# Kernel optimization log

Hardware: AMD Instinct MI355X
Metric: run time of the kernel (lower is better)

Reference implementation:

```python
import jax, jax.numpy as jnp
import numpy as np

N = 4096      # nodes
E = 65536     # edges
BAG = 16      # bloom indices per node
BF = 8192     # bloom_filter_dim (padding_idx == BF)
CIN = 128     # in_channels
HID = 512     # hidden_channels
G = 64        # num graphs
ALPHA = 0.2   # PPR teleport prob


def _prelu(z, a):
    return jnp.where(z >= 0, z, a * z)


def _mlp(x, W1, b1, W2, b2, W3, b3, a1, a2, a3, Ws, bs):
    h = _prelu(x @ W1 + b1, a1)
    h = _prelu(h @ W2 + b2, a2)
    h = _prelu(h @ W3 + b3, a3)
    return h + x @ Ws + bs


def setup_inputs() -> dict:
    key = jax.random.key(0)
    ks = iter(jax.random.split(key, 48))
    rn = lambda shape, s=0.05: jax.random.normal(next(ks), shape, dtype=jnp.float32) * s
    z = lambda *s: jnp.zeros(s, jnp.float32)
    inp = {}
    inp['codebook'] = rn((BF + 1, CIN)).at[BF].set(0.0)  # padding row zero
    # GCN tower 1
    inp['g1_W0'] = rn((CIN, HID)); inp['g1_b0'] = z(HID)
    inp['g1_W1'] = rn((HID, HID)); inp['g1_b1'] = z(HID)
    inp['g1_a'] = jnp.full((HID,), 0.25, jnp.float32)
    # GCN tower 2 (diffusion view)
    inp['g2_W0'] = rn((CIN, HID)); inp['g2_b0'] = z(HID)
    inp['g2_W1'] = rn((HID, HID)); inp['g2_b1'] = z(HID)
    inp['g2_a'] = jnp.full((HID,), 0.25, jnp.float32)
    # MLP1 (local, HID->HID)
    inp['m1_W1'] = rn((HID, HID)); inp['m1_b1'] = z(HID)
    inp['m1_W2'] = rn((HID, HID)); inp['m1_b2'] = z(HID)
    inp['m1_W3'] = rn((HID, HID)); inp['m1_b3'] = z(HID)
    inp['m1_a1'] = jnp.float32(0.25); inp['m1_a2'] = jnp.float32(0.25); inp['m1_a3'] = jnp.float32(0.25)
    inp['m1_Ws'] = rn((HID, HID)); inp['m1_bs'] = z(HID)
    # MLP2 (global, 2*HID -> HID)
    inp['m2_W1'] = rn((2 * HID, HID)); inp['m2_b1'] = z(HID)
    inp['m2_W2'] = rn((HID, HID)); inp['m2_b2'] = z(HID)
    inp['m2_W3'] = rn((HID, HID)); inp['m2_b3'] = z(HID)
    inp['m2_a1'] = jnp.float32(0.25); inp['m2_a2'] = jnp.float32(0.25); inp['m2_a3'] = jnp.float32(0.25)
    inp['m2_Ws'] = rn((2 * HID, HID)); inp['m2_bs'] = z(HID)
    inp['x_idx'] = jax.random.randint(next(ks), (N, BAG), 0, BF)
    inp['edge_index'] = jax.random.randint(next(ks), (2, E), 0, N)
    inp['batch'] = jnp.sort(jax.random.randint(next(ks), (N,), 0, G))
    return inp


def reference(codebook,
              g1_W0, g1_b0, g1_W1, g1_b1, g1_a,
              g2_W0, g2_b0, g2_W1, g2_b1, g2_a,
              m1_W1, m1_b1, m1_W2, m1_b2, m1_W3, m1_b3, m1_a1, m1_a2, m1_a3, m1_Ws, m1_bs,
              m2_W1, m2_b1, m2_W2, m2_b2, m2_W3, m2_b3, m2_a1, m2_a2, m2_a3, m2_Ws, m2_bs,
              x_idx, edge_index, batch):
    # EmbeddingBag (mean mode, padding_idx=BF)
    mask = (x_idx != BF)
    emb = codebook[x_idx]                                    # [N, BAG, CIN]
    x = (emb * mask[..., None]).sum(1) / jnp.maximum(mask.sum(1)[:, None], 1).astype(emb.dtype)
    src, dst = edge_index[0], edge_index[1]
    # --- sparse GCN normalization (self-loops, symmetric norm) ---
    sl = jnp.arange(N)
    s = jnp.concatenate([src, sl]); d = jnp.concatenate([dst, sl])
    deg = jax.ops.segment_sum(jnp.ones(s.shape[0], x.dtype), d, N)
    dis = 1.0 / jnp.sqrt(jnp.maximum(deg, 1e-12))
    nrm = (dis[s] * dis[d])[:, None]
    def gcn_sparse(z, W, b):
        return jax.ops.segment_sum((z @ W)[s] * nrm, d, N) + b
    # --- PPR diffusion: S = alpha*(I - (1-alpha) * D^-1/2 (A+I) D^-1/2)^-1 ---
    I = jnp.eye(N, dtype=x.dtype)
    A = jnp.zeros((N, N), x.dtype).at[src, dst].set(1.0)
    Ah = A + I
    di = 1.0 / jnp.sqrt(Ah.sum(1))
    An = di[:, None] * Ah * di[None, :]
    S = ALPHA * jnp.linalg.solve(I - (1.0 - ALPHA) * An, I)
    # GCN normalization of the dense diffusion graph (self-loop weight 1,
    # degrees over target nodes, messages flow row(src)->col(dst))
    Sh = S + I
    dc = 1.0 / jnp.sqrt(jnp.maximum(Sh.sum(0), 1e-12))
    P = dc[:, None] * Sh.T * dc[None, :]
    def gcn_dense(z, W, b):
        return P @ (z @ W) + b
    def tower(xin, gcn_fn, W0, b0, W1, b1, a):
        z1 = _prelu(gcn_fn(xin, W0, b0), a)
        z2 = _prelu(gcn_fn(z1, W1, b1), a)
        g = jnp.concatenate([jax.ops.segment_sum(z1, batch, G),
                             jax.ops.segment_sum(z2, batch, G)], axis=1)
        return z2, g
    lv1, gv1 = tower(x, gcn_sparse, g1_W0, g1_b0, g1_W1, g1_b1, g1_a)
    lv2, gv2 = tower(x, gcn_dense, g2_W0, g2_b0, g2_W1, g2_b1, g2_a)  # PPR view keeps x unchanged
    lv1 = _mlp(lv1, m1_W1, m1_b1, m1_W2, m1_b2, m1_W3, m1_b3, m1_a1, m1_a2, m1_a3, m1_Ws, m1_bs)
    lv2 = _mlp(lv2, m1_W1, m1_b1, m1_W2, m1_b2, m1_W3, m1_b3, m1_a1, m1_a2, m1_a3, m1_Ws, m1_bs)
    gv1 = _mlp(gv1, m2_W1, m2_b1, m2_W2, m2_b2, m2_W3, m2_b3, m2_a1, m2_a2, m2_a3, m2_Ws, m2_bs)
    gv2 = _mlp(gv2, m2_W1, m2_b1, m2_W2, m2_b2, m2_W3, m2_b3, m2_a1, m2_a2, m2_a3, m2_Ws, m2_bs)
    return (lv1, gv1, lv2, gv2)
```

## Files before the change

### kernel.cpp

```cpp
#include <hip/hip_runtime.h>

#define NN 4096
#define NE 65536
#define NBAG 16
#define BFD 8192
#define CIN 128
#define HIDC 512
#define NG 64
#define ALPHA_C 0.2f
#define BETA_C 0.8f
#define K_CH 10
#define K_W 10

typedef unsigned short u16;
typedef __attribute__((ext_vector_type(8))) short short8;
typedef __attribute__((ext_vector_type(4))) short short4v;
typedef __attribute__((ext_vector_type(4))) float f32x4;
typedef __attribute__((ext_vector_type(2))) float f32x2;

__device__ __forceinline__ short f2bf(float f){
  unsigned u = __float_as_uint(f);
  u += 0x7fffu + ((u >> 16) & 1u);
  return (short)(u >> 16);
}
__device__ __forceinline__ float bf2f(u16 h){
  return __uint_as_float(((unsigned)h) << 16);
}
__device__ __forceinline__ void gload16(const void* g, const void* l){
  __builtin_amdgcn_global_load_lds(
    (const __attribute__((address_space(1))) unsigned int*)g,
    (__attribute__((address_space(3))) unsigned int*)l, 16, 0, 0);
}

__global__ void k_prep0(const float* __restrict__ cb, const int* __restrict__ xidx,
                        float* __restrict__ xf, u16* __restrict__ xfbf,
                        const int* __restrict__ ei, unsigned* __restrict__ Ab,
                        unsigned* __restrict__ ATb, int* __restrict__ cntD,
                        const int* __restrict__ batch, int* __restrict__ bcnt){
  int bx = blockIdx.x;
  if (bx < 2048){
    int n = bx*2 + (threadIdx.x >> 7);
    int c = threadIdx.x & 127;
    float acc = 0.f; int cnt = 0;
    #pragma unroll
    for (int b = 0; b < NBAG; ++b){
      int id = xidx[n*NBAG + b];
      if (id != BFD){ acc += cb[(size_t)id*CIN + c]; ++cnt; }
    }
    float v = acc / (float)(cnt > 0 ? cnt : 1);
    xf[(size_t)n*CIN + c] = v;
    xfbf[(size_t)n*CIN + c] = (u16)f2bf(v);
  } else if (bx < 2304){
    int e = (bx - 2048)*256 + threadIdx.x;
    int s = ei[e], d = ei[NE + e];
    atomicOr(&Ab[s*128 + (d >> 5)], 1u << (d & 31));
    atomicOr(&ATb[d*128 + (s >> 5)], 1u << (s & 31));
    atomicAdd(&cntD[d], 1);
  } else {
    int n = (bx - 2304)*256 + threadIdx.x;
    if (n < NN) atomicAdd(&bcnt[batch[n]], 1);
  }
}

__global__ void k_popc2(const unsigned* __restrict__ Ab, const unsigned* __restrict__ ATb,
                        float* __restrict__ di, int* __restrict__ cntAT){
  int wid = (blockIdx.x*blockDim.x + threadIdx.x) >> 6;
  int lane = threadIdx.x & 63;
  if (wid >= 2*NN) return;
  const unsigned* bits; int r;
  if (wid < NN){ bits = Ab; r = wid; }
  else { bits = ATb; r = wid - NN; }
  int s = __popc(bits[r*128 + lane]) + __popc(bits[r*128 + 64 + lane]);
  #pragma unroll
  for (int off = 32; off > 0; off >>= 1) s += __shfl_down(s, off);
  if (lane == 0){
    if (wid < NN) di[r] = rsqrtf((float)s + 1.0f);
    else cntAT[r] = s;
  }
}

__global__ void k_prefix3(const int* __restrict__ c0, int* __restrict__ r0, int n0,
                          const int* __restrict__ c1, int* __restrict__ r1, int n1,
                          const int* __restrict__ c2, int* __restrict__ r2, int n2,
                          float* __restrict__ dis){
  const int* cnt; int* rp; int n;
  if (blockIdx.x == 0){ cnt = c0; rp = r0; n = n0; }
  else if (blockIdx.x == 1){ cnt = c1; rp = r1; n = n1; }
  else { cnt = c2; rp = r2; n = n2; }
  __shared__ int a[4096];
  __shared__ int ps[1024];
  int t = threadIdx.x;
  for (int i = t; i < 4096; i += 1024) a[i] = (i < n) ? cnt[i] : 0;
  __syncthreads();
  if (blockIdx.x == 1){
    for (int i = t; i < NN; i += 1024) dis[i] = rsqrtf((float)a[i] + 1.0f);
  }
  int b0 = a[t*4], b1 = a[t*4+1], b2 = a[t*4+2], b3 = a[t*4+3];
  int s0 = b0, s1 = s0+b1, s2 = s1+b2, s3 = s2+b3;
  ps[t] = s3;
  __syncthreads();
  for (int off = 1; off < 1024; off <<= 1){
    int v = ps[t];
    int u = (t >= off) ? ps[t-off] : 0;
    __syncthreads();
    ps[t] = v + u;
    __syncthreads();
  }
  int excl = (t > 0) ? ps[t-1] : 0;
  int base = t*4;
  if (base     < n) rp[base]   = excl;
  if (base + 1 < n) rp[base+1] = excl + s0;
  if (base + 2 < n) rp[base+2] = excl + s1;
  if (base + 3 < n) rp[base+3] = excl + s2;
  if (t == 1023) rp[n] = ps[1023];
}

struct WDesc { const float* src; u16* dst; int K; int N; };
struct WPack { WDesc w[12]; };

__global__ void k_fillwconv(const unsigned* __restrict__ bits, const int* __restrict__ rpA,
                            int* __restrict__ colidx,
                            const int* __restrict__ ei, const int* __restrict__ rpD,
                            int* __restrict__ cur, int* __restrict__ srcs,
                            WPack p){
  int bx = blockIdx.x;
  if (bx < 1024){
    int wid = (bx*blockDim.x + threadIdx.x) >> 6;
    int lane = threadIdx.x & 63;
    unsigned w0 = bits[wid*128 + lane];
    unsigned w1 = bits[wid*128 + 64 + lane];
    int c = __popc(w0) + __popc(w1);
    int x = c;
    #pragma unroll
    for (int d = 1; d < 64; d <<= 1){
      int y = __shfl_up(x, d);
      if (lane >= d) x += y;
    }
    int pos = rpA[wid] + (x - c);
    while (w0){ int b = __ffs(w0) - 1; w0 &= w0 - 1; colidx[pos++] = lane*32 + b; }
    while (w1){ int b = __ffs(w1) - 1; w1 &= w1 - 1; colidx[pos++] = (64 + lane)*32 + b; }
  } else if (bx < 1280){
    int e = (bx - 1024)*256 + threadIdx.x;
    int s = ei[e], d = ei[NE + e];
    int pos = atomicAdd(&cur[d], 1);
    srcs[rpD[d] + pos] = s;
  } else {
    int t5 = bx - 1280;
    int z = t5 >> 9;
    int rem = t5 & 511;
    int ky = rem >> 4, nx = rem & 15;
    WDesc d = p.w[z];
    int k0 = ky*32, n0 = nx*32;
    if (k0 >= d.K || n0 >= d.N) return;
    __shared__ float t[32][33];
    int tx = threadIdx.x & 31, ty = threadIdx.x >> 5;
    #pragma unroll
    for (int r = 0; r < 4; ++r){
      int row = ty + r*8;
      t[row][tx] = d.src[(size_t)(k0 + row)*d.N + n0 + tx];
    }
    __syncthreads();
    #pragma unroll
    for (int r = 0; r < 4; ++r){
      int row = ty + r*8;
      d.dst[(size_t)(n0 + row)*d.K + k0 + tx] = (u16)f2bf(t[tx][row]);
    }
  }
}

__global__ __launch_bounds__(256) void k_gcn_sp(const u16* __restrict__ U, float* __restrict__ out,
    u16* __restrict__ outbf,
    const int* __restrict__ rp, const int* __restrict__ srcs, const float* __restrict__ dis,
    const float* __restrict__ bias, const float* __restrict__ avec){
  int wid = (blockIdx.x*256 + threadIdx.x) >> 6;
  int lane = threadIdx.x & 63;
  if (wid >= NN) return;
  int j = wid;
  f32x4 a0 = {0,0,0,0}, a1 = {0,0,0,0};
  int b = rp[j], e = rp[j+1];
  for (int base = b; base < e; base += 64){
    int idx = base + lane;
    int myc = 0; float myd = 0.f;
    if (idx < e){ myc = srcs[idx]; myd = dis[myc]; }
    int m = min(64, e - base);
    for (int k = 0; k < m; ++k){
      int s = __shfl(myc, k); float w = __shfl(myd, k);
      const u16* Us = U + (size_t)s*HIDC;
      short4v q0 = *(const short4v*)(Us + lane*4);
      short4v q1 = *(const short4v*)(Us + 256 + lane*4);
      #pragma unroll
      for (int r = 0; r < 4; ++r){
        a0[r] += w*bf2f((u16)q0[r]);
        a1[r] += w*bf2f((u16)q1[r]);
      }
    }
  }
  float dj = dis[j];
  const u16* Uj = U + (size_t)j*HIDC;
  short4v s0 = *(const short4v*)(Uj + lane*4);
  short4v s1 = *(const short4v*)(Uj + 256 + lane*4);
  #pragma unroll
  for (int r = 0; r < 4; ++r){
    a0[r] += dj*bf2f((u16)s0[r]);
    a1[r] += dj*bf2f((u16)s1[r]);
  }
  float* op = out + (size_t)j*HIDC;
  u16* ob = outbf + (size_t)j*HIDC;
  #pragma unroll
  for (int v = 0; v < 4; ++v){
    int c0 = lane*4 + v, c1 = 256 + lane*4 + v;
    float x0 = dj*a0[v] + bias[c0]; float p0 = avec[c0];
    float r0 = x0 >= 0.f ? x0 : p0*x0;
    op[c0] = r0; ob[c0] = (u16)f2bf(r0);
    float x1 = dj*a1[v] + bias[c1]; float p1 = avec[c1];
    float r1 = x1 >= 0.f ? x1 : p1*x1;
    op[c1] = r1; ob[c1] = (u16)f2bf(r1);
  }
}

template<int MODE>
__global__ __launch_bounds__(256) void k_wstep(const float* __restrict__ w, const float* wp,
    float* __restrict__ wn, const int* __restrict__ rp, const int* __restrict__ cols,
    const float* __restrict__ di, float* __restrict__ dcv, float om,
    const float* __restrict__ xf, float* __restrict__ Zb128){
  int wid = (blockIdx.x*256 + threadIdx.x) >> 6;
  int lane = threadIdx.x & 63;
  if (wid >= NN) return;
  int b = rp[wid], e = rp[wid+1];
  float acc = 0.f;
  for (int k = b + lane; k < e; k += 64){
    int i = cols[k];
    float wi = (MODE == 0) ? ALPHA_C : w[i];
    acc += di[i]*wi;
  }
  #pragma unroll
  for (int o = 32; o > 0; o >>= 1) acc += __shfl_xor(acc, o);
  float dj = di[wid];
  float wj = (MODE == 0) ? ALPHA_C : w[wid];
  float basic = ALPHA_C + BETA_C*dj*(acc + dj*wj);
  float v = (MODE == 0) ? basic : (om*basic + (1.f - om)*wp[wid]);
  if (MODE == 2){
    float d2 = rsqrtf(fmaxf(v + 1.0f, 1e-12f));
    if (lane == 0) dcv[wid] = d2;
    f32x2 xv = *(const f32x2*)(xf + (size_t)wid*128 + lane*2);
    f32x2 z; z[0] = ALPHA_C*d2*xv[0]; z[1] = ALPHA_C*d2*xv[1];
    *(f32x2*)(Zb128 + (size_t)wid*128 + lane*2) = z;
  } else {
    if (lane == 0) wn[wid] = v;
  }
}

template<int FIN>
__global__ __launch_bounds__(256) void k_b128(const float* __restrict__ X, const float* __restrict__ Z,
    const float* Xp, float* Xn, u16* __restrict__ Pxbf,
    const int* __restrict__ rp, const int* __restrict__ cols,
    const float* __restrict__ di, float om,
    const float* __restrict__ dcv, const float* __restrict__ xf){
  int wid = (blockIdx.x*256 + threadIdx.x) >> 6;
  int lane = threadIdx.x & 63;
  if (wid >= NN) return;
  int j = wid;
  int b = rp[j], e = rp[j+1];
  float dj = di[j];
  f32x2 a0 = {0,0};
  for (int base = b; base < e; base += 64){
    int idx = base + lane;
    int myc = 0; float myd = 0.f;
    if (idx < e){ myc = cols[idx]; myd = di[myc]; }
    int m = min(64, e - base);
    for (int k = 0; k < m; ++k){
      int i = __shfl(myc, k); float w = __shfl(myd, k);
      a0 += w * (*(const f32x2*)(X + (size_t)i*128 + lane*2));
    }
  }
  a0 += dj * (*(const f32x2*)(X + (size_t)j*128 + lane*2));
  f32x2 basic = *(const f32x2*)(Z + (size_t)j*128 + lane*2) + (BETA_C*dj)*a0;
  f32x2 xp = *(const f32x2*)(Xp + (size_t)j*128 + lane*2);
  f32x2 v; v[0] = om*basic[0] + (1.f-om)*xp[0]; v[1] = om*basic[1] + (1.f-om)*xp[1];
  if constexpr (FIN){
    float d2 = dcv[j];
    f32x2 fv = *(const f32x2*)(xf + (size_t)j*128 + lane*2);
    unsigned pk = (unsigned)(unsigned short)f2bf(d2*(v[0] + d2*fv[0]))
                | ((unsigned)(unsigned short)f2bf(d2*(v[1] + d2*fv[1])) << 16);
    *(unsigned*)(Pxbf + (size_t)j*128 + lane*2) = pk;
  } else {
    *(f32x2*)(Xn + (size_t)j*128 + lane*2) = v;
  }
}

template<int FIN>
__global__ __launch_bounds__(256) void k_b512d(const float* __restrict__ X, const float* __restrict__ Z,
    const float* Xp, float* Xn, u16* __restrict__ Xnbf,
    const int* __restrict__ rp, const int* __restrict__ cols,
    const float* __restrict__ di, float om,
    const float* __restrict__ dcv, const u16* __restrict__ Ubf,
    const float* __restrict__ bias, const float* __restrict__ avec){
  int wid = (blockIdx.x*256 + threadIdx.x) >> 6;
  int lane = threadIdx.x & 63;
  if (wid >= NN) return;
  int b = rp[wid], e = rp[wid+1];
  float dj = di[wid];
  const int co0 = lane*4, co1 = 256 + lane*4;
  f32x4 a0 = {0,0,0,0}, a1 = {0,0,0,0};
  for (int base = b; base < e; base += 64){
    int idx = base + lane;
    int myc = 0; float myd = 0.f;
    if (idx < e){ myc = cols[idx]; myd = di[myc]; }
    int m = min(64, e - base);
    for (int k = 0; k < m; ++k){
      int i = __shfl(myc, k); float w = __shfl(myd, k);
      const float* Xi = X + (size_t)i*512;
      a0 += w * (*(const f32x4*)(Xi + co0));
      a1 += w * (*(const f32x4*)(Xi + co1));
    }
  }
  const float* Xj = X + (size_t)wid*512;
  a0 += dj * (*(const f32x4*)(Xj + co0));
  a1 += dj * (*(const f32x4*)(Xj + co1));
  const float* Zj = Z + (size_t)wid*512;
  f32x4 b0 = *(const f32x4*)(Zj + co0) + (BETA_C*dj)*a0;
  f32x4 b1 = *(const f32x4*)(Zj + co1) + (BETA_C*dj)*a1;
  const float* Pj = Xp + (size_t)wid*512;
  f32x4 p0 = *(const f32x4*)(Pj + co0);
  f32x4 p1 = *(const f32x4*)(Pj + co1);
  f32x4 v0, v1;
  #pragma unroll
  for (int q = 0; q < 4; ++q){
    v0[q] = om*b0[q] + (1.f-om)*p0[q];
    v1[q] = om*b1[q] + (1.f-om)*p1[q];
  }
  if constexpr (FIN){
    float d2 = dcv[wid];
    const u16* Uj = Ubf + (size_t)wid*512;
    short4v pk0, pk1;
    #pragma unroll
    for (int q = 0; q < 4; ++q){
      float x0 = d2*(v0[q] + d2*bf2f(Uj[co0 + q])) + bias[co0 + q];
      float pa0 = avec[co0 + q];
      float r0 = x0 >= 0.f ? x0 : pa0*x0;
      v0[q] = r0; pk0[q] = f2bf(r0);
      float x1 = d2*(v1[q] + d2*bf2f(Uj[co1 + q])) + bias[co1 + q];
      float pa1 = avec[co1 + q];
      float r1 = x1 >= 0.f ? x1 : pa1*x1;
      v1[q] = r1; pk1[q] = f2bf(r1);
    }
    float* oj = Xn + (size_t)wid*512;
    u16* bj = Xnbf + (size_t)wid*512;
    *(f32x4*)(oj + co0) = v0;
    *(f32x4*)(oj + co1) = v1;
    *(short4v*)(bj + co0) = pk0;
    *(short4v*)(bj + co1) = pk1;
  } else {
    float* oj = Xn + (size_t)wid*512;
    *(f32x4*)(oj + co0) = v0;
    *(f32x4*)(oj + co1) = v1;
  }
}

__global__ void k_segsum(const float* __restrict__ z1, const float* __restrict__ z2,
                         const int* __restrict__ gptr, u16* __restrict__ gv){
  int g = blockIdx.x, t = threadIdx.x;
  float s0 = 0, s1 = 0, s2 = 0, s3 = 0;
  int rb = gptr[g], re = gptr[g+1];
  for (int r = rb; r < re; ++r){
    s0 += z1[(size_t)r*HIDC + t];       s1 += z1[(size_t)r*HIDC + 256 + t];
    s2 += z2[(size_t)r*HIDC + t];       s3 += z2[(size_t)r*HIDC + 256 + t];
  }
  gv[g*1024 + t] = (u16)f2bf(s0); gv[g*1024 + 256 + t] = (u16)f2bf(s1);
  gv[g*1024 + 512 + t] = (u16)f2bf(s2); gv[g*1024 + 768 + t] = (u16)f2bf(s3);
}

template<int BM, int BN, int ACT, int ADDM, int BIAS, int KC, int SPLIT, int ZOUT, int WF32, int WBF, int DUAL>
__global__ __launch_bounds__(256, 2) void k_gemm(
    const u16* __restrict__ A, const u16* __restrict__ Bt,
    float* __restrict__ C, u16* __restrict__ Cb,
    const float* __restrict__ bias, const float* __restrict__ ap,
    const float* __restrict__ addm, float* __restrict__ C2,
    float* __restrict__ zb, const float* __restrict__ dcv,
    const float* __restrict__ bias2, const float* __restrict__ ap2,
    int M, int Nn, int K)
{
  __shared__ __align__(16) u16 As[2][BM*32];
  __shared__ __align__(16) u16 Bs[2][BN*32];
  const int tid = threadIdx.x;
  int nwg = gridDim.x * gridDim.y;
  int flat = blockIdx.y * gridDim.x + blockIdx.x;
  int swz = (flat & 7) * (nwg >> 3) + (flat >> 3);
  int bxx = swz % gridDim.x, byy = swz / gridDim.x;
  const int bm0 = byy*BM, bn0 = bxx*BN;
  const int lane = tid & 63, wv = tid >> 6;
  const int wr = wv >> 1, wc = wv & 1;
  constexpr int MR = BM/32, NR = BN/32;
  f32x4 acc[MR][NR];
  #pragma unroll
  for (int i = 0; i < MR; ++i)
    #pragma unroll
    for (int j = 0; j < NR; ++j) acc[i][j] = (f32x4){0.f,0.f,0.f,0.f};
  const int r0 = wr*(BM/2), c0 = wc*(BN/2);
  const int glr = lane >> 2, glc = (lane & 3)*8;
  int k0 = 0, k1 = K;
  if constexpr (KC > 0){ k0 = blockIdx.z*KC; k1 = k0 + KC; }
  const int nt = (k1 - k0) >> 5;
  auto STAGE = [&](int buf, int kt){
    #pragma unroll
    for (int q = 0; q < BM/64; ++q)
      gload16(A + (size_t)(bm0 + q*64 + wv*16 + glr)*K + kt + glc, &As[buf][(q*4+wv)*512]);
    #pragma unroll
    for (int q = 0; q < BN/64; ++q)
      gload16(Bt + (size_t)(bn0 + q*64 + wv*16 + glr)*K + kt + glc, &Bs[buf][(q*4+wv)*512]);
  };
  STAGE(0, k0);
  __syncthreads();
  for (int t = 0; t < nt; ++t){
    if (t + 1 < nt) STAGE((t+1)&1, k0 + ((t+1) << 5));
    short8 af[MR], bfv[NR];
    #pragma unroll
    for (int mi = 0; mi < MR; ++mi)
      af[mi] = *(const short8*)&As[t&1][(r0 + mi*16 + (lane & 15))*32 + (lane >> 4)*8];
    #pragma unroll
    for (int ni = 0; ni < NR; ++ni)
      bfv[ni] = *(const short8*)&Bs[t&1][(c0 + ni*16 + (lane & 15))*32 + (lane >> 4)*8];
    #pragma unroll
    for (int mi = 0; mi < MR; ++mi)
      #pragma unroll
      for (int ni = 0; ni < NR; ++ni)
        acc[mi][ni] = __builtin_amdgcn_mfma_f32_16x16x32_bf16(af[mi], bfv[ni], acc[mi][ni], 0, 0, 0);
    __syncthreads();
  }
  #pragma unroll
  for (int mi = 0; mi < MR; ++mi){
    #pragma unroll
    for (int ni = 0; ni < NR; ++ni){
      int col = bn0 + c0 + ni*16 + (lane & 15);
      #pragma unroll
      for (int q = 0; q < 4; ++q){
        int row = bm0 + r0 + mi*16 + ((lane >> 4) << 2) + q;
        float v = acc[mi][ni][q];
        if constexpr (KC > 0){
          C[(size_t)blockIdx.z*M*Nn + (size_t)row*Nn + col] = v;
        } else if constexpr (DUAL){
          if (col < 512){
            v += bias[col];
            C[(size_t)row*512 + col] = v;
          } else {
            int c2 = col - 512;
            v += bias2[c2];
            float a = ap2[0];
            v = v >= 0.f ? v : a*v;
            Cb[(size_t)row*512 + c2] = (u16)f2bf(v);
          }
        } else {
          if constexpr (BIAS) v += bias[col];
          if constexpr (ACT == 1){ float a = ap[col]; v = v >= 0.f ? v : a*v; }
          if constexpr (ACT == 2){ float a = ap[0];   v = v >= 0.f ? v : a*v; }
          if constexpr (ADDM) v += addm[(size_t)row*Nn + col];
          if constexpr (WF32){
            if constexpr (SPLIT){
              float* dst = (row < NN) ? (C + (size_t)row*Nn) : (C2 + (size_t)(row - NN)*Nn);
              dst[col] = v;
            } else {
              C[(size_t)row*Nn + col] = v;
            }
          }
          if constexpr (WBF) Cb[(size_t)row*Nn + col] = (u16)f2bf(v);
          if constexpr (ZOUT) zb[(size_t)row*Nn + col] = ALPHA_C * dcv[row] * v;
        }
      }
    }
  }
}

template<int MODE>
__global__ void k_red(const float* __restrict__ part, int KS, int Nn,
                      const float* __restrict__ b1, const float* __restrict__ a1s,
                      const float* __restrict__ b2, const float* __restrict__ a2s,
                      float* __restrict__ Cf, u16* __restrict__ Cb,
                      const float* __restrict__ addm,
                      float* __restrict__ o1, float* __restrict__ o2){
  int idx = blockIdx.x*256 + threadIdx.x;
  if (idx >= 128*Nn) return;
  float v = 0.f;
  for (int z = 0; z < KS; ++z) v += part[(size_t)z*128*Nn + idx];
  int row = idx / Nn, col = idx - row*Nn;
  if constexpr (MODE == 0){
    if (col < 512){
      v += b1[col];
      Cf[(size_t)row*512 + col] = v;
    } else {
      int c2 = col - 512;
      v += b2[c2];
      float a = a2s[0]; v = v >= 0.f ? v : a*v;
      Cb[(size_t)row*512 + c2] = (u16)f2bf(v);
    }
  } else if constexpr (MODE == 1){
    v += b1[col];
    float a = a1s[0]; v = v >= 0.f ? v : a*v;
    Cb[idx] = (u16)f2bf(v);
  } else {
    v += b1[col];
    float a = a1s[0]; v = v >= 0.f ? v : a*v;
    v += addm[idx];
    if (row < NG) o1[(size_t)row*Nn + col] = v;
    else o2[(size_t)(row - NG)*Nn + col] = v;
  }
}

extern "C" void kernel_launch(void* const* d_in, const int* in_sizes, int n_in,
                              void* d_out, int out_size, void* d_ws, size_t ws_size,
                              hipStream_t stream) {
  const float* cb   = (const float*)d_in[0];
  const float* g1W0 = (const float*)d_in[1];  const float* g1b0 = (const float*)d_in[2];
  const float* g1W1 = (const float*)d_in[3];  const float* g1b1 = (const float*)d_in[4];
  const float* g1a  = (const float*)d_in[5];
  const float* g2W0 = (const float*)d_in[6];  const float* g2b0 = (const float*)d_in[7];
  const float* g2W1 = (const float*)d_in[8];  const float* g2b1 = (const float*)d_in[9];
  const float* g2a  = (const float*)d_in[10];
  const float* m1W1 = (const float*)d_in[11]; const float* m1b1 = (const float*)d_in[12];
  const float* m1W2 = (const float*)d_in[13]; const float* m1b2 = (const float*)d_in[14];
  const float* m1W3 = (const float*)d_in[15]; const float* m1b3 = (const float*)d_in[16];
  const float* m1a1 = (const float*)d_in[17]; const float* m1a2 = (const float*)d_in[18];
  const float* m1a3 = (const float*)d_in[19];
  const float* m1Ws = (const float*)d_in[20]; const float* m1bs = (const float*)d_in[21];
  const float* m2W1 = (const float*)d_in[22]; const float* m2b1 = (const float*)d_in[23];
  const float* m2W2 = (const float*)d_in[24]; const float* m2b2 = (const float*)d_in[25];
  const float* m2W3 = (const float*)d_in[26]; const float* m2b3 = (const float*)d_in[27];
  const float* m2a1 = (const float*)d_in[28]; const float* m2a2 = (const float*)d_in[29];
  const float* m2a3 = (const float*)d_in[30];
  const float* m2Ws = (const float*)d_in[31]; const float* m2bs = (const float*)d_in[32];
  const int* xidx  = (const int*)d_in[33];
  const int* ei    = (const int*)d_in[34];
  const int* batch = (const int*)d_in[35];
  float* out = (float*)d_out;
  char* W = (char*)d_ws;
  constexpr size_t MB = 1024u*1024u;
  constexpr size_t KB = 1024u;

  unsigned* Abits  = (unsigned*)(W);
  unsigned* ATbits = (unsigned*)(W + 2*MB);
  u16* w_g1W0t   = (u16*)(W);
  u16* w_g2W0t   = (u16*)(W + 128*KB);
  u16* w_g1W1t   = (u16*)(W + 256*KB);
  u16* w_g2W1t   = (u16*)(W + 768*KB);
  u16* w_m1WsW1t = (u16*)(W + 1280*KB);
  u16* w_m1W2t   = (u16*)(W + 2304*KB);
  u16* w_m1W3t   = (u16*)(W + 2816*KB);
  char* M4 = W + 4*MB;
  int* cntD  = (int*)(M4);
  int* cur   = (int*)(M4 + 16*KB);
  int* bcnt  = (int*)(M4 + 32*KB);
  int* cntAT = (int*)(M4 + 48*KB);
  int* rpAT  = (int*)(M4 + 80*KB);
  int* rpD   = (int*)(M4 + 100*KB);
  int* gptr  = (int*)(M4 + 120*KB);
  float* di  = (float*)(M4 + 124*KB);
  float* dis = (float*)(M4 + 140*KB);
  float* dc  = (float*)(M4 + 156*KB);
  float* wv0 = (float*)(M4 + 172*KB);
  float* wv1 = (float*)(M4 + 188*KB);
  int* colAT = (int*)(W + 4*MB + 256*KB);
  int* srcD  = (int*)(W + 4*MB + 512*KB);
  u16* gvbf  = (u16*)(W + 4*MB + 768*KB);
  u16* gh1bf = (u16*)(W + 5*MB);
  u16* gh2bf = (u16*)(W + 5*MB + 128*KB);
  float* gsb = (float*)(W + 5*MB + 256*KB);
  float* xf  = (float*)(W + 6*MB);
  u16* xfbf  = (u16*)(W + 8*MB);
  u16* PxBf  = (u16*)(W + 9*MB);
  u16* w_m2WsW1t = (u16*)(W + 10*MB);
  u16* w_m2W2t   = (u16*)(W + 12*MB);
  u16* w_m2W3t   = (u16*)(W + 12*MB + 512*KB);
  float* Zb128 = (float*)(W + 13*MB);
  float* Zb  = (float*)(W + 15*MB);
  float* XA  = (float*)(W + 23*MB);
  float* XB  = (float*)(W + 31*MB);
  u16* z1sbf = (u16*)(W + 35*MB);
  u16* Ubf   = (u16*)(W + 39*MB);
  float* z1s = (float*)(W + 43*MB);
  u16* zsbf  = (u16*)(W + 51*MB);
  u16* z21bf = zsbf;
  u16* z22bf = (u16*)(W + 55*MB);
  float* ztmp = (float*)(W + 59*MB);
  float* sb  = Zb;
  u16* h1    = (u16*)(W + 31*MB);
  u16* h2    = (u16*)(W + 59*MB);
  float* gpart = (float*)(W + 59*MB);
  float* XA128 = XA;
  float* XB128 = XB;

  float omg[11];
  {
    double o = 1.0; omg[0] = 0.f; omg[1] = 1.0f;
    for (int k = 2; k <= 10; ++k){ o = 1.0/(1.0 - 0.16*o); omg[k] = (float)o; }
  }

  hipMemsetAsync(W, 0, 4*MB, stream);
  hipMemsetAsync(M4, 0, 64*KB, stream);

  k_prep0<<<2320, 256, 0, stream>>>(cb, xidx, xf, xfbf, ei, Abits, ATbits, cntD, batch, bcnt);
  k_popc2<<<2048, 256, 0, stream>>>(Abits, ATbits, di, cntAT);
  k_prefix3<<<3, 1024, 0, stream>>>(cntAT, rpAT, NN, cntD, rpD, NN, bcnt, gptr, NG, dis);
  {
    WPack p = {{ {g1W0, w_g1W0t, 128, 512}, {g2W0, w_g2W0t, 128, 512},
                 {g1W1, w_g1W1t, 512, 512}, {g2W1, w_g2W1t, 512, 512},
                 {m1Ws, w_m1WsW1t, 512, 512}, {m1W1, w_m1WsW1t + 512*512, 512, 512},
                 {m1W2, w_m1W2t, 512, 512}, {m1W3, w_m1W3t, 512, 512},
                 {m2Ws, w_m2WsW1t, 1024, 512}, {m2W1, w_m2WsW1t + 512*1024, 1024, 512},
                 {m2W2, w_m2W2t, 512, 512}, {m2W3, w_m2W3t, 512, 512} }};
    k_fillwconv<<<1280 + 6144, 256, 0, stream>>>(ATbits, rpAT, colAT, ei, rpD, cur, srcD, p);
  }

  k_gemm<128,64,0,0,0,0,0,0,0,1,0><<<dim3(8, 32), 256, 0, stream>>>(
      xfbf, w_g1W0t, nullptr, Ubf, nullptr, nullptr, nullptr, nullptr, nullptr, nullptr, nullptr, nullptr, NN, HIDC, CIN);
  k_gcn_sp<<<1024, 256, 0, stream>>>(Ubf, z1s, z1sbf, rpD, srcD, dis, g1b0, g1a);
  k_gemm<128,64,0,0,0,0,0,0,0,1,0><<<dim3(8, 32), 256, 0, stream>>>(
      z1sbf, w_g1W1t, nullptr, Ubf, nullptr, nullptr, nullptr, nullptr, nullptr, nullptr, nullptr, nullptr, NN, HIDC, HIDC);
  k_gcn_sp<<<1024, 256, 0, stream>>>(Ubf, ztmp, z21bf, rpD, srcD, dis, g1b1, g1a);
  k_segsum<<<NG, 256, 0, stream>>>(z1s, ztmp, gptr, gvbf);

  k_wstep<0><<<1024, 256, 0, stream>>>(nullptr, nullptr, wv0, rpAT, colAT, di, nullptr, 1.0f, nullptr, nullptr);
  {
    float *curp = wv0, *prv = wv0;
    for (int k = 2; k < K_W; ++k){
      float* nxt = (k == 2) ? wv1 : (float*)prv;
      if (k == 2) prv = wv0;
      k_wstep<1><<<1024, 256, 0, stream>>>(curp, prv, nxt, rpAT, colAT, di, nullptr, omg[k], nullptr, nullptr);
      float* t = curp; curp = nxt; prv = t;
    }
    k_wstep<2><<<1024, 256, 0, stream>>>(curp, prv, nullptr, rpAT, colAT, di, dc, omg[K_W], xf, Zb128);
  }

  k_b128<0><<<1024, 256, 0, stream>>>(Zb128, Zb128, Zb128, XA128, nullptr, rpAT, colAT, di, 1.0f, nullptr, nullptr);
  {
    float *curp = XA128, *prv = Zb128;
    for (int k = 2; k < K_CH; ++k){
      float* nxt = (k == 2) ? XB128 : prv;
      k_b128<0><<<1024, 256, 0, stream>>>(curp, Zb128, prv, nxt, nullptr, rpAT, colAT, di, omg[k], nullptr, nullptr);
      prv = curp; curp = nxt;
    }
    k_b128<1><<<1024, 256, 0, stream>>>(curp, Zb128, prv, nullptr, PxBf, rpAT, colAT, di, omg[K_CH], dc, xf);
  }
  k_gemm<128,64,1,0,1,0,0,0,1,1,0><<<dim3(8, 32), 256, 0, stream>>>(
      PxBf, w_g2W0t, z1s, z1sbf, g2b0, g2a, nullptr, nullptr, nullptr, nullptr, nullptr, nullptr, NN, HIDC, CIN);

  k_gemm<128,64,0,0,0,0,0,1,0,1,0><<<dim3(8, 32), 256, 0, stream>>>(
      z1sbf, w_g2W1t, nullptr, Ubf, nullptr, nullptr, nullptr, nullptr, Zb, dc, nullptr, nullptr, NN, HIDC, HIDC);
  k_b512d<0><<<1024, 256, 0, stream>>>(Zb, Zb, Zb, XA, nullptr, rpAT, colAT, di, 1.0f, nullptr, nullptr, nullptr, nullptr);
  {
    float *curp = XA, *prv = Zb;
    for (int k = 2; k < K_CH; ++k){
      float* nxt = (k == 2) ? XB : prv;
      k_b512d<0><<<1024, 256, 0, stream>>>(curp, Zb, prv, nxt, nullptr, rpAT, colAT, di, omg[k], nullptr, nullptr, nullptr, nullptr);
      prv = curp; curp = nxt;
    }
    k_b512d<1><<<1024, 256, 0, stream>>>(curp, Zb, prv, ztmp, z22bf, rpAT, colAT, di, omg[K_CH], dc, Ubf, g2b1, g2a);
  }
  k_segsum<<<NG, 256, 0, stream>>>(z1s, ztmp, gptr, gvbf + 64*1024);

  k_gemm<128,64,0,0,0,0,0,0,0,0,1><<<dim3(16, 64), 256, 0, stream>>>(
      zsbf, w_m1WsW1t, sb, h1, m1bs, nullptr, nullptr, nullptr, nullptr, nullptr, m1b1, m1a1, 8192, 1024, HIDC);
  k_gemm<128,64,2,0,1,0,0,0,0,1,0><<<dim3(8, 64), 256, 0, stream>>>(
      h1, w_m1W2t, nullptr, h2, m1b2, m1a2, nullptr, nullptr, nullptr, nullptr, nullptr, nullptr, 8192, HIDC, HIDC);
  k_gemm<128,64,2,1,1,0,1,0,1,0,0><<<dim3(8, 64), 256, 0, stream>>>(
      h2, w_m1W3t, out, nullptr, m1b3, m1a3, sb, out + 2129920, nullptr, nullptr, nullptr, nullptr, 8192, HIDC, HIDC);

  k_gemm<64,64,0,0,0,128,0,0,1,0,0><<<dim3(16, 2, 8), 256, 0, stream>>>(
      gvbf, w_m2WsW1t, gpart, nullptr, nullptr, nullptr, nullptr, nullptr, nullptr, nullptr, nullptr, nullptr, 128, 1024, 1024);
  k_red<0><<<512, 256, 0, stream>>>(gpart, 8, 1024, m2bs, nullptr, m2b1, m2a1, gsb, gh1bf, nullptr, nullptr, nullptr);
  k_gemm<64,64,0,0,0,64,0,0,1,0,0><<<dim3(8, 2, 8), 256, 0, stream>>>(
      gh1bf, w_m2W2t, gpart, nullptr, nullptr, nullptr, nullptr, nullptr, nullptr, nullptr, nullptr, nullptr, 128, HIDC, HIDC);
  k_red<1><<<256, 256, 0, stream>>>(gpart, 8, 512, m2b2, m2a2, nullptr, nullptr, nullptr, gh2bf, nullptr, nullptr, nullptr);
  k_gemm<64,64,0,0,0,64,0,0,1,0,0><<<dim3(8, 2, 8), 256, 0, stream>>>(
      gh2bf, w_m2W3t, gpart, nullptr, nullptr, nullptr, nullptr, nullptr, nullptr, nullptr, nullptr, nullptr, 128, HIDC, HIDC);
  k_red<2><<<256, 256, 0, stream>>>(gpart, 8, 512, m2b3, m2a3, nullptr, nullptr, nullptr, nullptr, gsb, out + 2097152, out + 4227072);
}
```

Measured before the change: 537.5 us.

## Store 512-wide PPR diffusion iterates in bf16 and fuse global MLP into one kernel

The 512-channel PPR/Chebyshev diffusion loop now reads and writes its neighbour-gathered iterates in bf16 instead of fp32. This halves the bandwidth of the dominant sparse gather passes, at the cost of extra rounding on every iteration. Separately, the global-view MLP, previously three split-K GEMMs plus three reduction kernels, is replaced by a single fused kernel. That kernel chains all three layers through shared memory, which removes five launches and the partial-sum round trips. Because it runs on only 8 blocks, it may underuse the GPU.

```diff
diff --git a/kernel.cpp b/kernel.cpp
--- a/kernel.cpp
+++ b/kernel.cpp
@@ -289,8 +289,8 @@
 }
 
 template<int FIN>
-__global__ __launch_bounds__(256) void k_b512d(const float* __restrict__ X, const float* __restrict__ Z,
-    const float* Xp, float* Xn, u16* __restrict__ Xnbf,
+__global__ __launch_bounds__(256) void k_b512h(const u16* __restrict__ X, const float* __restrict__ Z,
+    const u16* Xp, u16* Xn, float* __restrict__ zo, u16* __restrict__ zobf,
     const int* __restrict__ rp, const int* __restrict__ cols,
     const float* __restrict__ di, float om,
     const float* __restrict__ dcv, const u16* __restrict__ Ubf,
@@ -309,25 +309,37 @@
     int m = min(64, e - base);
     for (int k = 0; k < m; ++k){
       int i = __shfl(myc, k); float w = __shfl(myd, k);
-      const float* Xi = X + (size_t)i*512;
-      a0 += w * (*(const f32x4*)(Xi + co0));
-      a1 += w * (*(const f32x4*)(Xi + co1));
-    }
-  }
-  const float* Xj = X + (size_t)wid*512;
-  a0 += dj * (*(const f32x4*)(Xj + co0));
-  a1 += dj * (*(const f32x4*)(Xj + co1));
+      const u16* Xi = X + (size_t)i*512;
+      short4v x0 = *(const short4v*)(Xi + co0);
+      short4v x1 = *(const short4v*)(Xi + co1);
+      #pragma unroll
+      for (int q = 0; q < 4; ++q){
+        a0[q] += w*bf2f((u16)x0[q]);
+        a1[q] += w*bf2f((u16)x1[q]);
+      }
+    }
+  }
+  {
+    const u16* Xj = X + (size_t)wid*512;
+    short4v x0 = *(const short4v*)(Xj + co0);
+    short4v x1 = *(const short4v*)(Xj + co1);
+    #pragma unroll
+    for (int q = 0; q < 4; ++q){
+      a0[q] += dj*bf2f((u16)x0[q]);
+      a1[q] += dj*bf2f((u16)x1[q]);
+    }
+  }
   const float* Zj = Z + (size_t)wid*512;
   f32x4 b0 = *(const f32x4*)(Zj + co0) + (BETA_C*dj)*a0;
   f32x4 b1 = *(const f32x4*)(Zj + co1) + (BETA_C*dj)*a1;
-  const float* Pj = Xp + (size_t)wid*512;
-  f32x4 p0 = *(const f32x4*)(Pj + co0);
-  f32x4 p1 = *(const f32x4*)(Pj + co1);
+  const u16* Pj = Xp + (size_t)wid*512;
+  short4v p0 = *(const short4v*)(Pj + co0);
+  short4v p1 = *(const short4v*)(Pj + co1);
   f32x4 v0, v1;
   #pragma unroll
   for (int q = 0; q < 4; ++q){
-    v0[q] = om*b0[q] + (1.f-om)*p0[q];
-    v1[q] = om*b1[q] + (1.f-om)*p1[q];
+    v0[q] = om*b0[q] + (1.f-om)*bf2f((u16)p0[q]);
+    v1[q] = om*b1[q] + (1.f-om)*bf2f((u16)p1[q]);
   }
   if constexpr (FIN){
     float d2 = dcv[wid];
@@ -344,16 +356,19 @@
       float r1 = x1 >= 0.f ? x1 : pa1*x1;
       v1[q] = r1; pk1[q] = f2bf(r1);
     }
-    float* oj = Xn + (size_t)wid*512;
-    u16* bj = Xnbf + (size_t)wid*512;
+    float* oj = zo + (size_t)wid*512;
+    u16* bj = zobf + (size_t)wid*512;
     *(f32x4*)(oj + co0) = v0;
     *(f32x4*)(oj + co1) = v1;
     *(short4v*)(bj + co0) = pk0;
     *(short4v*)(bj + co1) = pk1;
   } else {
-    float* oj = Xn + (size_t)wid*512;
-    *(f32x4*)(oj + co0) = v0;
-    *(f32x4*)(oj + co1) = v1;
+    short4v w0, w1;
+    #pragma unroll
+    for (int q = 0; q < 4; ++q){ w0[q] = f2bf(v0[q]); w1[q] = f2bf(v1[q]); }
+    u16* oj = Xn + (size_t)wid*512;
+    *(short4v*)(oj + co0) = w0;
+    *(short4v*)(oj + co1) = w1;
   }
 }
 
@@ -370,13 +385,125 @@
   gv[g*1024 + 512 + t] = (u16)f2bf(s2); gv[g*1024 + 768 + t] = (u16)f2bf(s3);
 }
 
+__global__ __launch_bounds__(512) void k_mlp2(
+    const u16* __restrict__ gv, const u16* __restrict__ wsw1,
+    const u16* __restrict__ w2t, const u16* __restrict__ w3t,
+    const float* __restrict__ bs, const float* __restrict__ b1,
+    const float* __restrict__ b2, const float* __restrict__ b3,
+    const float* __restrict__ a1s, const float* __restrict__ a2s,
+    const float* __restrict__ a3s,
+    float* __restrict__ o1, float* __restrict__ o2)
+{
+  __shared__ __align__(16) u16 Ar[16*1032];
+  __shared__ float gsb_s[16*512];
+  __shared__ __align__(16) u16 h1_s[16*520];
+  __shared__ __align__(16) u16 h2_s[16*520];
+  int tid = threadIdx.x;
+  int wv = tid >> 6, lane = tid & 63;
+  int row0 = blockIdx.x * 16;
+  for (int c = tid; c < 2048; c += 512){
+    int r = c >> 7, i = (c & 127)*8;
+    *(short8*)&Ar[r*1032 + i] = *(const short8*)&gv[(size_t)(row0 + r)*1024 + i];
+  }
+  __syncthreads();
+  const int fr = lane & 15, fq = lane >> 4;
+  {
+    f32x4 acc[8];
+    #pragma unroll
+    for (int t = 0; t < 8; ++t) acc[t] = (f32x4){0,0,0,0};
+    for (int ks = 0; ks < 32; ++ks){
+      short8 af = *(const short8*)&Ar[fr*1032 + ks*32 + fq*8];
+      #pragma unroll
+      for (int t = 0; t < 8; ++t){
+        int n = (wv*8 + t)*16 + fr;
+        short8 bfv = *(const short8*)&wsw1[(size_t)n*1024 + ks*32 + fq*8];
+        acc[t] = __builtin_amdgcn_mfma_f32_16x16x32_bf16(af, bfv, acc[t], 0, 0, 0);
+      }
+    }
+    #pragma unroll
+    for (int t = 0; t < 8; ++t){
+      int n = (wv*8 + t)*16 + fr;
+      #pragma unroll
+      for (int q = 0; q < 4; ++q){
+        int r = fq*4 + q;
+        float v = acc[t][q];
+        if (n < 512){
+          gsb_s[r*512 + n] = v + bs[n];
+        } else {
+          float x = v + b1[n - 512];
+          float a = a1s[0];
+          x = x >= 0.f ? x : a*x;
+          h1_s[r*520 + (n - 512)] = (u16)f2bf(x);
+        }
+      }
+    }
+  }
+  __syncthreads();
+  {
+    f32x4 acc[4];
+    #pragma unroll
+    for (int t = 0; t < 4; ++t) acc[t] = (f32x4){0,0,0,0};
+    for (int ks = 0; ks < 16; ++ks){
+      short8 af = *(const short8*)&h1_s[fr*520 + ks*32 + fq*8];
+      #pragma unroll
+      for (int t = 0; t < 4; ++t){
+        int n = (wv*4 + t)*16 + fr;
+        short8 bfv = *(const short8*)&w2t[(size_t)n*512 + ks*32 + fq*8];
+        acc[t] = __builtin_amdgcn_mfma_f32_16x16x32_bf16(af, bfv, acc[t], 0, 0, 0);
+      }
+    }
+    #pragma unroll
+    for (int t = 0; t < 4; ++t){
+      int n = (wv*4 + t)*16 + fr;
+      #pragma unroll
+      for (int q = 0; q < 4; ++q){
+        int r = fq*4 + q;
+        float x = acc[t][q] + b2[n];
+        float a = a2s[0];
+        x = x >= 0.f ? x : a*x;
+        h2_s[r*520 + n] = (u16)f2bf(x);
+      }
+    }
+  }
+  __syncthreads();
+  {
+    f32x4 acc[4];
+    #pragma unroll
+    for (int t = 0; t < 4; ++t) acc[t] = (f32x4){0,0,0,0};
+    for (int ks = 0; ks < 16; ++ks){
+      short8 af = *(const short8*)&h2_s[fr*520 + ks*32 + fq*8];
+      #pragma unroll
+      for (int t = 0; t < 4; ++t){
+        int n = (wv*4 + t)*16 + fr;
+        short8 bfv = *(const short8*)&w3t[(size_t)n*512 + ks*32 + fq*8];
+        acc[t] = __builtin_amdgcn_mfma_f32_16x16x32_bf16(af, bfv, acc[t], 0, 0, 0);
+      }
+    }
+    #pragma unroll
+    for (int t = 0; t < 4; ++t){
+      int n = (wv*4 + t)*16 + fr;
+      #pragma unroll
+      for (int q = 0; q < 4; ++q){
+        int r = fq*4 + q;
+        float x = acc[t][q] + b3[n];
+        float a = a3s[0];
+        x = x >= 0.f ? x : a*x;
+        x += gsb_s[r*512 + n];
+        int grow = row0 + r;
+        if (grow < NG) o1[(size_t)grow*512 + n] = x;
+        else o2[(size_t)(grow - NG)*512 + n] = x;
+      }
+    }
+  }
+}
+
 template<int BM, int BN, int ACT, int ADDM, int BIAS, int KC, int SPLIT, int ZOUT, int WF32, int WBF, int DUAL>
 __global__ __launch_bounds__(256, 2) void k_gemm(
     const u16* __restrict__ A, const u16* __restrict__ Bt,
     float* __restrict__ C, u16* __restrict__ Cb,
     const float* __restrict__ bias, const float* __restrict__ ap,
     const float* __restrict__ addm, float* __restrict__ C2,
-    float* __restrict__ zb, const float* __restrict__ dcv,
+    float* __restrict__ zb, u16* __restrict__ zbh, const float* __restrict__ dcv,
     const float* __restrict__ bias2, const float* __restrict__ ap2,
     int M, int Nn, int K)
 {
@@ -463,45 +590,14 @@
             }
           }
           if constexpr (WBF) Cb[(size_t)row*Nn + col] = (u16)f2bf(v);
-          if constexpr (ZOUT) zb[(size_t)row*Nn + col] = ALPHA_C * dcv[row] * v;
+          if constexpr (ZOUT){
+            float zv = ALPHA_C * dcv[row] * v;
+            zb[(size_t)row*Nn + col] = zv;
+            zbh[(size_t)row*Nn + col] = (u16)f2bf(zv);
+          }
         }
       }
     }
-  }
-}
-
-template<int MODE>
-__global__ void k_red(const float* __restrict__ part, int KS, int Nn,
-                      const float* __restrict__ b1, const float* __restrict__ a1s,
-                      const float* __restrict__ b2, const float* __restrict__ a2s,
-                      float* __restrict__ Cf, u16* __restrict__ Cb,
-                      const float* __restrict__ addm,
-                      float* __restrict__ o1, float* __restrict__ o2){
-  int idx = blockIdx.x*256 + threadIdx.x;
-  if (idx >= 128*Nn) return;
-  float v = 0.f;
-  for (int z = 0; z < KS; ++z) v += part[(size_t)z*128*Nn + idx];
-  int row = idx / Nn, col = idx - row*Nn;
-  if constexpr (MODE == 0){
-    if (col < 512){
-      v += b1[col];
-      Cf[(size_t)row*512 + col] = v;
-    } else {
-      int c2 = col - 512;
-      v += b2[c2];
-      float a = a2s[0]; v = v >= 0.f ? v : a*v;
-      Cb[(size_t)row*512 + c2] = (u16)f2bf(v);
-    }
-  } else if constexpr (MODE == 1){
-    v += b1[col];
-    float a = a1s[0]; v = v >= 0.f ? v : a*v;
-    Cb[idx] = (u16)f2bf(v);
-  } else {
-    v += b1[col];
-    float a = a1s[0]; v = v >= 0.f ? v : a*v;
-    v += addm[idx];
-    if (row < NG) o1[(size_t)row*Nn + col] = v;
-    else o2[(size_t)(row - NG)*Nn + col] = v;
   }
 }
 
@@ -560,9 +656,6 @@
   int* colAT = (int*)(W + 4*MB + 256*KB);
   int* srcD  = (int*)(W + 4*MB + 512*KB);
   u16* gvbf  = (u16*)(W + 4*MB + 768*KB);
-  u16* gh1bf = (u16*)(W + 5*MB);
-  u16* gh2bf = (u16*)(W + 5*MB + 128*KB);
-  float* gsb = (float*)(W + 5*MB + 256*KB);
   float* xf  = (float*)(W + 6*MB);
   u16* xfbf  = (u16*)(W + 8*MB);
   u16* PxBf  = (u16*)(W + 9*MB);
@@ -571,9 +664,12 @@
   u16* w_m2W3t   = (u16*)(W + 12*MB + 512*KB);
   float* Zb128 = (float*)(W + 13*MB);
   float* Zb  = (float*)(W + 15*MB);
-  float* XA  = (float*)(W + 23*MB);
-  float* XB  = (float*)(W + 31*MB);
+  float* XA128 = (float*)(W + 23*MB);
+  float* XB128 = (float*)(W + 25*MB);
+  u16* Zbh  = (u16*)(W + 27*MB);
+  u16* XAh  = (u16*)(W + 31*MB);
   u16* z1sbf = (u16*)(W + 35*MB);
+  u16* XBh  = (u16*)(W + 35*MB);
   u16* Ubf   = (u16*)(W + 39*MB);
   float* z1s = (float*)(W + 43*MB);
   u16* zsbf  = (u16*)(W + 51*MB);
@@ -583,9 +679,6 @@
   float* sb  = Zb;
   u16* h1    = (u16*)(W + 31*MB);
   u16* h2    = (u16*)(W + 59*MB);
-  float* gpart = (float*)(W + 59*MB);
-  float* XA128 = XA;
-  float* XB128 = XB;
 
   float omg[11];
   {
@@ -610,10 +703,10 @@
   }
 
   k_gemm<128,64,0,0,0,0,0,0,0,1,0><<<dim3(8, 32), 256, 0, stream>>>(
-      xfbf, w_g1W0t, nullptr, Ubf, nullptr, nullptr, nullptr, nullptr, nullptr, nullptr, nullptr, nullptr, NN, HIDC, CIN);
+      xfbf, w_g1W0t, nullptr, Ubf, nullptr, nullptr, nullptr, nullptr, nullptr, nullptr, nullptr, nullptr, nullptr, NN, HIDC, CIN);
   k_gcn_sp<<<1024, 256, 0, stream>>>(Ubf, z1s, z1sbf, rpD, srcD, dis, g1b0, g1a);
   k_gemm<128,64,0,0,0,0,0,0,0,1,0><<<dim3(8, 32), 256, 0, stream>>>(
-      z1sbf, w_g1W1t, nullptr, Ubf, nullptr, nullptr, nullptr, nullptr, nullptr, nullptr, nullptr, nullptr, NN, HIDC, HIDC);
+      z1sbf, w_g1W1t, nullptr, Ubf, nullptr, nullptr, nullptr, nullptr, nullptr, nullptr, nullptr, nullptr, nullptr, NN, HIDC, HIDC);
   k_gcn_sp<<<1024, 256, 0, stream>>>(Ubf, ztmp, z21bf, rpD, srcD, dis, g1b1, g1a);
   k_segsum<<<NG, 256, 0, stream>>>(z1s, ztmp, gptr, gvbf);
 
@@ -640,36 +733,30 @@
     k_b128<1><<<1024, 256, 0, stream>>>(curp, Zb128, prv, nullptr, PxBf, rpAT, colAT, di, omg[K_CH], dc, xf);
   }
   k_gemm<128,64,1,0,1,0,0,0,1,1,0><<<dim3(8, 32), 256, 0, stream>>>(
-      PxBf, w_g2W0t, z1s, z1sbf, g2b0, g2a, nullptr, nullptr, nullptr, nullptr, nullptr, nullptr, NN, HIDC, CIN);
+      PxBf, w_g2W0t, z1s, z1sbf, g2b0, g2a, nullptr, nullptr, nullptr, nullptr, nullptr, nullptr, nullptr, NN, HIDC, CIN);
 
   k_gemm<128,64,0,0,0,0,0,1,0,1,0><<<dim3(8, 32), 256, 0, stream>>>(
-      z1sbf, w_g2W1t, nullptr, Ubf, nullptr, nullptr, nullptr, nullptr, Zb, dc, nullptr, nullptr, NN, HIDC, HIDC);
-  k_b512d<0><<<1024, 256, 0, stream>>>(Zb, Zb, Zb, XA, nullptr, rpAT, colAT, di, 1.0f, nullptr, nullptr, nullptr, nullptr);
-  {
-    float *curp = XA, *prv = Zb;
+      z1sbf, w_g2W1t, nullptr, Ubf, nullptr, nullptr, nullptr, nullptr, Zb, Zbh, dc, nullptr, nullptr, NN, HIDC, HIDC);
+  k_b512h<0><<<1024, 256, 0, stream>>>(Zbh, Zb, Zbh, XAh, nullptr, nullptr, rpAT, colAT, di, 1.0f, nullptr, nullptr, nullptr, nullptr);
+  {
+    u16 *curp = XAh, *prv = Zbh;
     for (int k = 2; k < K_CH; ++k){
-      float* nxt = (k == 2) ? XB : prv;
-      k_b512d<0><<<1024, 256, 0, stream>>>(curp, Zb, prv, nxt, nullptr, rpAT, colAT, di, omg[k], nullptr, nullptr, nullptr, nullptr);
+      u16* nxt = (k == 2) ? XBh : prv;
+      k_b512h<0><<<1024, 256, 0, stream>>>(curp, Zb, prv, nxt, nullptr, nullptr, rpAT, colAT, di, omg[k], nullptr, nullptr, nullptr, nullptr);
       prv = curp; curp = nxt;
     }
-    k_b512d<1><<<1024, 256, 0, stream>>>(curp, Zb, prv, ztmp, z22bf, rpAT, colAT, di, omg[K_CH], dc, Ubf, g2b1, g2a);
+    k_b512h<1><<<1024, 256, 0, stream>>>(curp, Zb, prv, nullptr, ztmp, z22bf, rpAT, colAT, di, omg[K_CH], dc, Ubf, g2b1, g2a);
   }
   k_segsum<<<NG, 256, 0, stream>>>(z1s, ztmp, gptr, gvbf + 64*1024);
 
   k_gemm<128,64,0,0,0,0,0,0,0,0,1><<<dim3(16, 64), 256, 0, stream>>>(
-      zsbf, w_m1WsW1t, sb, h1, m1bs, nullptr, nullptr, nullptr, nullptr, nullptr, m1b1, m1a1, 8192, 1024, HIDC);
+      zsbf, w_m1WsW1t, sb, h1, m1bs, nullptr, nullptr, nullptr, nullptr, nullptr, nullptr, m1b1, m1a1, 8192, 1024, HIDC);
   k_gemm<128,64,2,0,1,0,0,0,0,1,0><<<dim3(8, 64), 256, 0, stream>>>(
-      h1, w_m1W2t, nullptr, h2, m1b2, m1a2, nullptr, nullptr, nullptr, nullptr, nullptr, nullptr, 8192, HIDC, HIDC);
+      h1, w_m1W2t, nullptr, h2, m1b2, m1a2, nullptr, nullptr, nullptr, nullptr, nullptr, nullptr, nullptr, 8192, HIDC, HIDC);
   k_gemm<128,64,2,1,1,0,1,0,1,0,0><<<dim3(8, 64), 256, 0, stream>>>(
-      h2, w_m1W3t, out, nullptr, m1b3, m1a3, sb, out + 2129920, nullptr, nullptr, nullptr, nullptr, 8192, HIDC, HIDC);
-
-  k_gemm<64,64,0,0,0,128,0,0,1,0,0><<<dim3(16, 2, 8), 256, 0, stream>>>(
-      gvbf, w_m2WsW1t, gpart, nullptr, nullptr, nullptr, nullptr, nullptr, nullptr, nullptr, nullptr, nullptr, 128, 1024, 1024);
-  k_red<0><<<512, 256, 0, stream>>>(gpart, 8, 1024, m2bs, nullptr, m2b1, m2a1, gsb, gh1bf, nullptr, nullptr, nullptr);
-  k_gemm<64,64,0,0,0,64,0,0,1,0,0><<<dim3(8, 2, 8), 256, 0, stream>>>(
-      gh1bf, w_m2W2t, gpart, nullptr, nullptr, nullptr, nullptr, nullptr, nullptr, nullptr, nullptr, nullptr, 128, HIDC, HIDC);
-  k_red<1><<<256, 256, 0, stream>>>(gpart, 8, 512, m2b2, m2a2, nullptr, nullptr, nullptr, gh2bf, nullptr, nullptr, nullptr);
-  k_gemm<64,64,0,0,0,64,0,0,1,0,0><<<dim3(8, 2, 8), 256, 0, stream>>>(
-      gh2bf, w_m2W3t, gpart, nullptr, nullptr, nullptr, nullptr, nullptr, nullptr, nullptr, nullptr, nullptr, 128, HIDC, HIDC);
-  k_red<2><<<256, 256, 0, stream>>>(gpart, 8, 512, m2b3, m2a3, nullptr, nullptr, nullptr, nullptr, gsb, out + 2097152, out + 4227072);
-}
+      h2, w_m1W3t, out, nullptr, m1b3, m1a3, sb, out + 2129920, nullptr, nullptr, nullptr, nullptr, nullptr, 8192, HIDC, HIDC);
+
+  k_mlp2<<<8, 512, 0, stream>>>(gvbf, w_m2WsW1t, w_m2W2t, w_m2W3t,
+      m2bs, m2b1, m2b2, m2b3, m2a1, m2a2, m2a3,
+      out + 2097152, out + 4227072);
+}
```

Result: slower. 578.4 us (+7.6%).
